# Kernel optimization log

Hardware: AMD Instinct MI355X
Metric: run time of the kernel (lower is better)

## Reference

```python
import jax, jax.numpy as jnp
import numpy as np

EMBED_DIM = 1024
NUM_HEADS = 16
HEAD_DIM = EMBED_DIM // NUM_HEADS
MAX_DIST = 128
NUM_BUCKETS = 2 * MAX_DIST + 1  # 257: fixes off-by-one in original Embedding sizing


def setup_inputs() -> dict:
    key = jax.random.key(0)
    ks = jax.random.split(key, 10)
    B, S, D = 2, 2048, EMBED_DIM
    s = 1.0 / np.sqrt(D)
    return {
        "x": jax.random.normal(ks[0], (B, S, D), dtype=jnp.float32),
        "Wq": jax.random.normal(ks[1], (D, D), dtype=jnp.float32) * s,
        "bq": jnp.zeros((D,), dtype=jnp.float32),
        "Wk": jax.random.normal(ks[2], (D, D), dtype=jnp.float32) * s,
        "bk": jnp.zeros((D,), dtype=jnp.float32),
        "Wv": jax.random.normal(ks[3], (D, D), dtype=jnp.float32) * s,
        "bv": jnp.zeros((D,), dtype=jnp.float32),
        "Wo": jax.random.normal(ks[4], (D, D), dtype=jnp.float32) * s,
        "bo": jnp.zeros((D,), dtype=jnp.float32),
        "rel_emb": jax.random.normal(ks[5], (NUM_BUCKETS, NUM_HEADS), dtype=jnp.float32) * 0.02,
    }


def _rel_bias(rel_emb, seq_len):
    # relative position clamped to [-MAX_DIST, MAX_DIST], shifted to [0, 2*MAX_DIST]
    pos = jnp.arange(seq_len)
    rel = jnp.clip(pos[:, None] - pos[None, :], -MAX_DIST, MAX_DIST) + MAX_DIST
    bias = rel_emb[rel]                    # [S, S, H]
    return jnp.transpose(bias, (2, 0, 1))  # [H, S, S]


def reference(x, Wq, bq, Wk, bk, Wv, bv, Wo, bo, rel_emb):
    B, S, D = x.shape
    H, Hd = NUM_HEADS, HEAD_DIM
    # torch Linear: y = x @ W.T + b
    q = (x @ Wq.T + bq).reshape(B, S, H, Hd).transpose(0, 2, 1, 3)  # [B,H,S,Hd]
    k = (x @ Wk.T + bk).reshape(B, S, H, Hd).transpose(0, 2, 1, 3)
    v = (x @ Wv.T + bv).reshape(B, S, H, Hd).transpose(0, 2, 1, 3)
    scores = jnp.einsum("bhqd,bhkd->bhqk", q, k) / jnp.sqrt(jnp.float32(Hd))
    scores = scores + _rel_bias(rel_emb, S)[None]  # add [H,S,S] bias
    probs = jax.nn.softmax(scores, axis=-1)
    out = jnp.einsum("bhqk,bhkd->bhqd", probs, v)
    out = out.transpose(0, 2, 1, 3).reshape(B, S, D)
    return out @ Wo.T + bo
```

## Files before the change

kernel.cpp:

```cpp
#include <hip/hip_runtime.h>
#include <hip/hip_bf16.h>
#include <cstdint>
#include <cstddef>

#define DEVI __device__ __forceinline__

static constexpr int SEQ = 2048;
static constexpr int DM  = 1024;
static constexpr int NH  = 16;
static constexpr int HD  = 64;
static constexpr int NTOK = 2 * SEQ;
static constexpr int NBUCKET = 257;
static constexpr float LOG2E = 1.44269504088896f;

typedef __attribute__((ext_vector_type(8))) short bf16x8;
typedef __attribute__((ext_vector_type(4))) float f32x4;
#define MFMA16(a, b, c) __builtin_amdgcn_mfma_f32_16x16x32_bf16((a), (b), (c), 0, 0, 0)

DEVI float bf1(uint16_t u)  { return __uint_as_float(((uint32_t)u) << 16); }
DEVI uint16_t f2bf(float f) {
    uint32_t x = __float_as_uint(f);
    x += 0x7fffu + ((x >> 16) & 1u);
    return (uint16_t)(x >> 16);
}
DEVI bf16x8 ld_frag(const uint16_t* p) {
    union { uint4 u; bf16x8 f; } c;
    c.u = *(const uint4*)p;
    return c.f;
}
DEVI void gld16(const uint16_t* g, uint16_t* l) {
    __builtin_amdgcn_global_load_lds(
        (const __attribute__((address_space(1))) uint32_t*)g,
        (__attribute__((address_space(3))) uint32_t*)l, 16, 0, 0);
}

__global__ void sniff_kernel(const uint16_t* __restrict__ x, int* __restrict__ flag)
{
    int bad = 0;
    for (int i = threadIdx.x; i < 512; i += 64) {
        const float v = bf1(x[i]);
        if (!(fabsf(v) < 64.0f)) bad = 1;
    }
    const unsigned long long m = __ballot(bad);
    if (threadIdx.x == 0) *flag = (m != 0ull) ? 1 : 0;
}

__global__ __launch_bounds__(256)
void convert_kernel(const void* __restrict__ x, const void* __restrict__ Wq,
                    const void* __restrict__ Wk, const void* __restrict__ Wv,
                    const void* __restrict__ Wo, const void* __restrict__ bq,
                    const void* __restrict__ bk, const void* __restrict__ bv,
                    const void* __restrict__ bo, uint16_t* __restrict__ dst,
                    const int* __restrict__ flagp)
{
    const bool f32in = (*flagp != 0);
    const size_t M4 = 4194304, M1 = 1048576;
    const size_t e = ((size_t)blockIdx.x * 256 + threadIdx.x) * 8;
    const void* src; size_t off;
    if      (e < M4)                 { src = x;  off = e; }
    else if (e < M4 + M1)            { src = Wq; off = e - M4; }
    else if (e < M4 + 2*M1)          { src = Wk; off = e - M4 - M1; }
    else if (e < M4 + 3*M1)          { src = Wv; off = e - M4 - 2*M1; }
    else if (e < M4 + 4*M1)          { src = Wo; off = e - M4 - 3*M1; }
    else if (e < M4 + 4*M1 + 1024)   { src = bq; off = e - M4 - 4*M1; }
    else if (e < M4 + 4*M1 + 2048)   { src = bk; off = e - M4 - 4*M1 - 1024; }
    else if (e < M4 + 4*M1 + 3072)   { src = bv; off = e - M4 - 4*M1 - 2048; }
    else                             { src = bo; off = e - M4 - 4*M1 - 3072; }
    if (f32in) {
        const float4 a = *(const float4*)((const float*)src + off);
        const float4 b = *(const float4*)((const float*)src + off + 4);
        uint4 o;
        o.x = (uint32_t)f2bf(a.x) | ((uint32_t)f2bf(a.y) << 16);
        o.y = (uint32_t)f2bf(a.z) | ((uint32_t)f2bf(a.w) << 16);
        o.z = (uint32_t)f2bf(b.x) | ((uint32_t)f2bf(b.y) << 16);
        o.w = (uint32_t)f2bf(b.z) | ((uint32_t)f2bf(b.w) << 16);
        *(uint4*)(dst + e) = o;
    } else {
        *(uint4*)(dst + e) = *(const uint4*)((const uint16_t*)src + off);
    }
}

__global__ __launch_bounds__(256)
void gemm_qkv(const uint16_t* __restrict__ xc, const uint16_t* __restrict__ Wqkv,
              const uint16_t* __restrict__ bqkv,
              uint16_t* __restrict__ Qw, uint16_t* __restrict__ Kw,
              uint16_t* __restrict__ Vt)
{
    __shared__ uint16_t As[128 * 32];
    __shared__ uint16_t Bs[128 * 32];
    const int tid = threadIdx.x, bx = blockIdx.x;
    const int lane = tid & 63, wave = tid >> 6;
    const int ln = lane & 15, quad = lane >> 4;
    const int wm = (wave & 1) * 64, wn = (wave >> 1) * 64;

    const uint16_t *Ab, *Bb;
    int bm, bn, vor;
    if (bx < 512) {
        vor = 0; bm = (bx >> 4) * 128; bn = (bx & 15) * 128;
        Ab = xc + (size_t)bm * DM;  Bb = Wqkv + (size_t)bn * DM;
    } else {
        vor = 1; const int b2 = bx - 512; bm = (b2 >> 5) * 128; bn = (b2 & 31) * 128;
        Ab = Wqkv + (size_t)(2048 + bm) * DM;  Bb = xc + (size_t)bn * DM;
    }

    f32x4 acc[4][4];
    #pragma unroll
    for (int i = 0; i < 4; ++i)
        #pragma unroll
        for (int j = 0; j < 4; ++j) acc[i][j] = (f32x4){0.f, 0.f, 0.f, 0.f};

    const int s0 = tid, s1 = 256 + tid;
    const uint16_t* ga0 = Ab + (size_t)(s0 >> 2) * DM + (s0 & 3) * 8;
    const uint16_t* ga1 = Ab + (size_t)(s1 >> 2) * DM + (s1 & 3) * 8;
    const uint16_t* gb0 = Bb + (size_t)(s0 >> 2) * DM + (s0 & 3) * 8;
    const uint16_t* gb1 = Bb + (size_t)(s1 >> 2) * DM + (s1 & 3) * 8;

    for (int k0 = 0; k0 < DM; k0 += 32) {
        __syncthreads();
        gld16(ga0 + k0, &As[s0 * 8]);
        gld16(ga1 + k0, &As[s1 * 8]);
        gld16(gb0 + k0, &Bs[s0 * 8]);
        gld16(gb1 + k0, &Bs[s1 * 8]);
        __syncthreads();

        bf16x8 af[4], bfr[4];
        #pragma unroll
        for (int t = 0; t < 4; ++t) {
            af[t]  = ld_frag(&As[(wm + t * 16 + ln) * 32 + quad * 8]);
            bfr[t] = ld_frag(&Bs[(wn + t * 16 + ln) * 32 + quad * 8]);
        }
        #pragma unroll
        for (int ti = 0; ti < 4; ++ti)
            #pragma unroll
            for (int tj = 0; tj < 4; ++tj)
                acc[ti][tj] = MFMA16(af[ti], bfr[tj], acc[ti][tj]);
    }

    if (!vor) {
        #pragma unroll
        for (int tj = 0; tj < 4; ++tj) {
            const int c = bn + wn + tj * 16 + ln;
            const int mat = c >> 10, h = (c >> 6) & 15, hd = c & 63;
            uint16_t* dstp = mat ? Kw : Qw;
            const float scale = mat ? 1.0f : (0.125f * LOG2E);
            const float bb = bf1(bqkv[c]);
            #pragma unroll
            for (int ti = 0; ti < 4; ++ti)
                #pragma unroll
                for (int r = 0; r < 4; ++r) {
                    const int row = bm + wm + ti * 16 + quad * 4 + r;
                    const int b = row >> 11, s = row & 2047;
                    dstp[(((size_t)b * NH + h) * SEQ + s) * HD + hd] =
                        f2bf((acc[ti][tj][r] + bb) * scale);
                }
        }
    } else {
        #pragma unroll
        for (int ti = 0; ti < 4; ++ti)
            #pragma unroll
            for (int r = 0; r < 4; ++r) {
                const int f = bm + wm + ti * 16 + quad * 4 + r;
                const int h = f >> 6, hd = f & 63;
                const float bb = bf1(bqkv[2048 + f]);
                #pragma unroll
                for (int tj = 0; tj < 4; ++tj) {
                    const int t = bn + wn + tj * 16 + ln;
                    const int b = t >> 11, s = t & 2047;
                    Vt[(((size_t)b * NH + h) * HD + hd) * SEQ + s] = f2bf(acc[ti][tj][r] + bb);
                }
            }
    }
}

__global__ __launch_bounds__(256)
void gemm_out(const uint16_t* __restrict__ Cw, const uint16_t* __restrict__ Woc,
              const uint16_t* __restrict__ boc, void* __restrict__ out,
              const int* __restrict__ flagp)
{
    __shared__ uint16_t As[128 * 32];
    __shared__ uint16_t Bs[64 * 32];
    const int tid = threadIdx.x, bx = blockIdx.x;
    const int lane = tid & 63, wave = tid >> 6;
    const int ln = lane & 15, quad = lane >> 4;
    const int wm = (wave & 1) * 64, wn = (wave >> 1) * 32;
    const int bm = (bx >> 4) * 128, bn = (bx & 15) * 64;
    const uint16_t* Ab = Cw + (size_t)bm * DM;
    const uint16_t* Bb = Woc + (size_t)bn * DM;

    f32x4 acc[4][2];
    #pragma unroll
    for (int i = 0; i < 4; ++i)
        #pragma unroll
        for (int j = 0; j < 2; ++j) acc[i][j] = (f32x4){0.f, 0.f, 0.f, 0.f};

    const int s0 = tid, s1 = 256 + tid;
    const uint16_t* ga0 = Ab + (size_t)(s0 >> 2) * DM + (s0 & 3) * 8;
    const uint16_t* ga1 = Ab + (size_t)(s1 >> 2) * DM + (s1 & 3) * 8;
    const uint16_t* gb0 = Bb + (size_t)(s0 >> 2) * DM + (s0 & 3) * 8;

    for (int k0 = 0; k0 < DM; k0 += 32) {
        __syncthreads();
        gld16(ga0 + k0, &As[s0 * 8]);
        gld16(ga1 + k0, &As[s1 * 8]);
        gld16(gb0 + k0, &Bs[s0 * 8]);
        __syncthreads();

        bf16x8 af[4], bfr[2];
        #pragma unroll
        for (int t = 0; t < 4; ++t)
            af[t] = ld_frag(&As[(wm + t * 16 + ln) * 32 + quad * 8]);
        #pragma unroll
        for (int t = 0; t < 2; ++t)
            bfr[t] = ld_frag(&Bs[(wn + t * 16 + ln) * 32 + quad * 8]);
        #pragma unroll
        for (int ti = 0; ti < 4; ++ti)
            #pragma unroll
            for (int tj = 0; tj < 2; ++tj)
                acc[ti][tj] = MFMA16(af[ti], bfr[tj], acc[ti][tj]);
    }

    const bool f32o = (*flagp != 0);
    #pragma unroll
    for (int tj = 0; tj < 2; ++tj) {
        const int c = bn + wn + tj * 16 + ln;
        const float bb = bf1(boc[c]);
        #pragma unroll
        for (int ti = 0; ti < 4; ++ti)
            #pragma unroll
            for (int r = 0; r < 4; ++r) {
                const int row = bm + wm + ti * 16 + quad * 4 + r;
                const float v = acc[ti][tj][r] + bb;
                if (f32o) ((float*)out)[(size_t)row * DM + c] = v;
                else      ((uint16_t*)out)[(size_t)row * DM + c] = f2bf(v);
            }
    }
}

#define ATTN_COMPUTE(K0, KSB, VSB)                                             \
  do {                                                                         \
    const int mode_ = ((K0) >= q0 + 256) ? 0 : (((K0) + 192 <= q0) ? 2 : 1);   \
    if (mode_ != 1) {                                                          \
      const float binit_ = (mode_ == 0) ? bneg : bpos;                         \
      _Pragma("unroll")                                                        \
      for (int nt = 0; nt < 4; ++nt) {                                         \
        const bf16x8 kf0 = ld_frag((KSB) + kvo[nt][0]);                        \
        const bf16x8 kf1 = ld_frag((KSB) + kvo[nt][1]);                        \
        f32x4 s4 = (f32x4){binit_, binit_, binit_, binit_};                    \
        s4 = MFMA16(kf0, qf0, s4);                                             \
        s4 = MFMA16(kf1, qf1, s4);                                             \
        uint32_t pb[4];                                                        \
        _Pragma("unroll")                                                      \
        for (int r = 0; r < 4; ++r)                                            \
          pb[r] = __float_as_uint(__builtin_amdgcn_exp2f(s4[r]));              \
        const uint2 dw = {__builtin_amdgcn_perm(pb[1], pb[0], 0x07060302u),    \
                          __builtin_amdgcn_perm(pb[3], pb[2], 0x07060302u)};   \
        *(uint2*)Pw[nt] = dw;                                                  \
      }                                                                        \
    } else {                                                                   \
      const int iq_ = q0 + wave * 16 + ln + 128 - (K0) - quad * 4;             \
      _Pragma("unroll")                                                        \
      for (int nt = 0; nt < 4; ++nt) {                                         \
        const bf16x8 kf0 = ld_frag((KSB) + kvo[nt][0]);                        \
        const bf16x8 kf1 = ld_frag((KSB) + kvo[nt][1]);                        \
        f32x4 s4 = (f32x4){0.f, 0.f, 0.f, 0.f};                                \
        s4 = MFMA16(kf0, qf0, s4);                                             \
        s4 = MFMA16(kf1, qf1, s4);                                             \
        uint32_t pb[4];                                                        \
        _Pragma("unroll")                                                      \
        for (int r = 0; r < 4; ++r) {                                          \
          int x_ = iq_ - (nt * 16 + r);                                        \
          x_ = max(0, min(256, x_));                                           \
          pb[r] = __float_as_uint(__builtin_amdgcn_exp2f(s4[r] + bias_s[x_])); \
        }                                                                      \
        const uint2 dw = {__builtin_amdgcn_perm(pb[1], pb[0], 0x07060302u),    \
                          __builtin_amdgcn_perm(pb[3], pb[2], 0x07060302u)};   \
        *(uint2*)Pw[nt] = dw;                                                  \
      }                                                                        \
    }                                                                          \
    const bf16x8 pf0 = ld_frag(pfp0);                                          \
    const bf16x8 pf1 = ld_frag(pfp1);                                          \
    lf = MFMA16(pf0, onef, lf);                                                \
    lf = MFMA16(pf1, onef, lf);                                                \
    _Pragma("unroll")                                                          \
    for (int dt = 0; dt < 4; ++dt) {                                           \
      o[dt] = MFMA16(pf0, ld_frag((VSB) + kvo[dt][0]), o[dt]);                 \
      o[dt] = MFMA16(pf1, ld_frag((VSB) + kvo[dt][1]), o[dt]);                 \
    }                                                                          \
  } while (0)

__global__ __launch_bounds__(512, 4)
void attn_mfma(const uint16_t* __restrict__ Q, const uint16_t* __restrict__ K,
               const uint16_t* __restrict__ Vt, const void* __restrict__ rel,
               uint16_t* __restrict__ ctx, const int* __restrict__ flagp)
{
    __shared__ alignas(16) uint16_t Ks[2][64 * 64];
    __shared__ alignas(16) uint16_t Vls[2][64 * 64];
    __shared__ alignas(16) uint16_t Pl[8][16 * 64];
    __shared__ float bias_s[NBUCKET];

    const bool f32in = (*flagp != 0);
    const int tid = threadIdx.x, wave = tid >> 6, lane = tid & 63;
    const int ln = lane & 15, quad = lane >> 4;

    const int blk = blockIdx.x;
    const int bh = (blk & 7) * 4 + ((blk >> 3) & 3);
    const int qt = blk >> 5;
    const int b = bh >> 4, h = bh & 15;
    const int q0 = qt * 128;

    const float C8 = 8.0f * LOG2E;
    for (int i = tid; i < NBUCKET; i += 512) {
        const float bv = f32in ? ((const float*)rel)[i * NH + h]
                               : bf1(((const uint16_t*)rel)[i * NH + h]);
        bias_s[i] = bv * LOG2E - C8;
    }

    const uint16_t* qp = Q + ((size_t)bh * SEQ + q0 + wave * 16 + ln) * HD;
    const bf16x8 qf0 = ld_frag(qp + quad * 8);
    const bf16x8 qf1 = ld_frag(qp + 32 + quad * 8);

    union { uint4 u; bf16x8 f; } onec;
    onec.u = (uint4){0x3F803F80u, 0x3F803F80u, 0x3F803F80u, 0x3F803F80u};
    const bf16x8 onef = onec.f;

    f32x4 o[4];
    f32x4 lf = (f32x4){0.f, 0.f, 0.f, 0.f};
    #pragma unroll
    for (int dt = 0; dt < 4; ++dt) o[dt] = (f32x4){0.f, 0.f, 0.f, 0.f};

    const int swz = ln & 7;
    uint16_t* myP = Pl[wave];

    const int r_ = tid >> 3, c_ = (tid & 7) ^ (r_ & 7);
    const int koff = r_ * HD + c_ * 8;
    const int voff = r_ * SEQ + c_ * 8;
    uint16_t* const kd0 = &Ks[0][tid * 8];
    uint16_t* const kd1 = &Ks[1][tid * 8];
    uint16_t* const vd0 = &Vls[0][tid * 8];
    uint16_t* const vd1 = &Vls[1][tid * 8];

    const uint16_t* kg = K  + (size_t)bh * SEQ * HD + koff;
    const uint16_t* vg = Vt + (size_t)bh * HD * SEQ + voff;

    int kvo[4][2];
    #pragma unroll
    for (int t = 0; t < 4; ++t) {
        const int row = (t * 16 + ln) * 64;
        kvo[t][0] = row + ((0 + quad) ^ swz) * 8;
        kvo[t][1] = row + ((4 + quad) ^ swz) * 8;
    }
    uint16_t* Pw[4];
    #pragma unroll
    for (int nt = 0; nt < 4; ++nt) {
        const int cb = (2 * nt + (quad >> 1)) ^ swz;
        Pw[nt] = &myP[ln * 64 + cb * 8 + (quad & 1) * 4];
    }
    const uint16_t* const pfp0 = &myP[ln * 64 + ((0 + quad) ^ swz) * 8];
    const uint16_t* const pfp1 = &myP[ln * 64 + ((4 + quad) ^ swz) * 8];

    gld16(kg, kd0); gld16(vg, vd0);
    kg += 64 * HD; vg += 64;
    __syncthreads();
    const float bneg = bias_s[0], bpos = bias_s[256];

    for (int t = 0; t < 16; ++t) {
        gld16(kg, kd1); gld16(vg, vd1);
        kg += 64 * HD; vg += 64;
        ATTN_COMPUTE(t * 128, &Ks[0][0], &Vls[0][0]);
        __syncthreads();

        if (t < 15) {
            gld16(kg, kd0); gld16(vg, vd0);
            kg += 64 * HD; vg += 64;
        }
        ATTN_COMPUTE(t * 128 + 64, &Ks[1][0], &Vls[1][0]);
        __syncthreads();
    }

    #pragma unroll
    for (int r = 0; r < 4; ++r) {
        const float inv = 1.0f / lf[r];
        const int qq = q0 + wave * 16 + quad * 4 + r;
        #pragma unroll
        for (int dt = 0; dt < 4; ++dt)
            ctx[(((size_t)b * SEQ + qq) * NH + h) * HD + dt * 16 + ln] =
                f2bf(o[dt][r] * inv);
    }
}

extern "C" void kernel_launch(void* const* d_in, const int* in_sizes, int n_in,
                              void* d_out, int out_size, void* d_ws, size_t ws_size,
                              hipStream_t stream)
{
    const void* x   = d_in[0];
    const void* Wq  = d_in[1];
    const void* bq  = d_in[2];
    const void* Wk  = d_in[3];
    const void* bk  = d_in[4];
    const void* Wv  = d_in[5];
    const void* bv  = d_in[6];
    const void* Wo  = d_in[7];
    const void* bo  = d_in[8];
    const void* rel = d_in[9];

    const size_t M4 = 4194304, M1 = 1048576;
    uint16_t* ws16 = (uint16_t*)d_ws;
    uint16_t* xc   = ws16;
    uint16_t* Wqkv = ws16 + M4;
    uint16_t* Woc  = ws16 + M4 + 3 * M1;
    uint16_t* bqkv = ws16 + M4 + 4 * M1;
    uint16_t* boc  = bqkv + 3072;
    uint16_t* Qw   = ws16 + M4 + 4 * M1 + 8192;
    uint16_t* Kw   = Qw + M4;
    uint16_t* Vt   = Kw + M4;
    int* flag = (int*)(Vt + M4);
    uint16_t* Cw = xc;

    sniff_kernel<<<1, 64, 0, stream>>>((const uint16_t*)x, flag);
    convert_kernel<<<4098, 256, 0, stream>>>(x, Wq, Wk, Wv, Wo, bq, bk, bv, bo,
                                             ws16, flag);
    gemm_qkv<<<768, 256, 0, stream>>>(xc, Wqkv, bqkv, Qw, Kw, Vt);
    attn_mfma<<<512, 512, 0, stream>>>(Qw, Kw, Vt, rel, Cw, flag);
    gemm_out<<<512, 256, 0, stream>>>(Cw, Woc, boc, d_out, flag);
}
```

Baseline: 207.4 us.

## Process two query sub-tiles per wave to reuse K/V fragments in attention

The attention block drops from 8 waves to 4, and each wave now handles 32 query rows as two 16-row groups. Every K and V fragment read from shared memory feeds two MFMAs instead of one, which halves LDS fragment traffic per unit of work. Each thread now issues two global-to-LDS copies per tile, since fewer threads remain to stage it. The cost is roughly double the accumulator and Q registers per wave and fewer waves per block, which may reduce latency hiding.

```diff
diff --git a/kernel.cpp b/kernel.cpp
--- a/kernel.cpp
+++ b/kernel.cpp
@@ -245,57 +245,72 @@
       for (int nt = 0; nt < 4; ++nt) {                                         \
         const bf16x8 kf0 = ld_frag((KSB) + kvo[nt][0]);                        \
         const bf16x8 kf1 = ld_frag((KSB) + kvo[nt][1]);                        \
-        f32x4 s4 = (f32x4){binit_, binit_, binit_, binit_};                    \
-        s4 = MFMA16(kf0, qf0, s4);                                             \
-        s4 = MFMA16(kf1, qf1, s4);                                             \
-        uint32_t pb[4];                                                        \
         _Pragma("unroll")                                                      \
-        for (int r = 0; r < 4; ++r)                                            \
-          pb[r] = __float_as_uint(__builtin_amdgcn_exp2f(s4[r]));              \
-        const uint2 dw = {__builtin_amdgcn_perm(pb[1], pb[0], 0x07060302u),    \
-                          __builtin_amdgcn_perm(pb[3], pb[2], 0x07060302u)};   \
-        *(uint2*)Pw[nt] = dw;                                                  \
+        for (int qg = 0; qg < 2; ++qg) {                                       \
+          f32x4 s4 = (f32x4){binit_, binit_, binit_, binit_};                  \
+          s4 = MFMA16(kf0, qf0[qg], s4);                                       \
+          s4 = MFMA16(kf1, qf1[qg], s4);                                       \
+          uint32_t pb[4];                                                      \
+          _Pragma("unroll")                                                    \
+          for (int r = 0; r < 4; ++r)                                          \
+            pb[r] = __float_as_uint(__builtin_amdgcn_exp2f(s4[r]));            \
+          const uint2 dw = {__builtin_amdgcn_perm(pb[1], pb[0], 0x07060302u),  \
+                            __builtin_amdgcn_perm(pb[3], pb[2], 0x07060302u)}; \
+          *(uint2*)Pw[qg][nt] = dw;                                            \
+        }                                                                      \
       }                                                                        \
     } else {                                                                   \
-      const int iq_ = q0 + wave * 16 + ln + 128 - (K0) - quad * 4;             \
       _Pragma("unroll")                                                        \
       for (int nt = 0; nt < 4; ++nt) {                                         \
         const bf16x8 kf0 = ld_frag((KSB) + kvo[nt][0]);                        \
         const bf16x8 kf1 = ld_frag((KSB) + kvo[nt][1]);                        \
-        f32x4 s4 = (f32x4){0.f, 0.f, 0.f, 0.f};                                \
-        s4 = MFMA16(kf0, qf0, s4);                                             \
-        s4 = MFMA16(kf1, qf1, s4);                                             \
-        uint32_t pb[4];                                                        \
         _Pragma("unroll")                                                      \
-        for (int r = 0; r < 4; ++r) {                                          \
-          int x_ = iq_ - (nt * 16 + r);                                        \
-          x_ = max(0, min(256, x_));                                           \
-          pb[r] = __float_as_uint(__builtin_amdgcn_exp2f(s4[r] + bias_s[x_])); \
+        for (int qg = 0; qg < 2; ++qg) {                                       \
+          const int iq_ = q0 + wave * 32 + qg * 16 + ln + 128 - (K0) - quad * 4;\
+          f32x4 s4 = (f32x4){0.f, 0.f, 0.f, 0.f};                              \
+          s4 = MFMA16(kf0, qf0[qg], s4);                                       \
+          s4 = MFMA16(kf1, qf1[qg], s4);                                       \
+          uint32_t pb[4];                                                      \
+          _Pragma("unroll")                                                    \
+          for (int r = 0; r < 4; ++r) {                                        \
+            int x_ = iq_ - (nt * 16 + r);                                      \
+            x_ = max(0, min(256, x_));                                         \
+            pb[r] = __float_as_uint(__builtin_amdgcn_exp2f(s4[r] + bias_s[x_]));\
+          }                                                                    \
+          const uint2 dw = {__builtin_amdgcn_perm(pb[1], pb[0], 0x07060302u),  \
+                            __builtin_amdgcn_perm(pb[3], pb[2], 0x07060302u)}; \
+          *(uint2*)Pw[qg][nt] = dw;                                            \
         }                                                                      \
-        const uint2 dw = {__builtin_amdgcn_perm(pb[1], pb[0], 0x07060302u),    \
-                          __builtin_amdgcn_perm(pb[3], pb[2], 0x07060302u)};   \
-        *(uint2*)Pw[nt] = dw;                                                  \
       }                                                                        \
     }                                                                          \
-    const bf16x8 pf0 = ld_frag(pfp0);                                          \
-    const bf16x8 pf1 = ld_frag(pfp1);                                          \
-    lf = MFMA16(pf0, onef, lf);                                                \
-    lf = MFMA16(pf1, onef, lf);                                                \
+    bf16x8 pfa[2], pfb[2];                                                     \
+    _Pragma("unroll")                                                          \
+    for (int qg = 0; qg < 2; ++qg) {                                           \
+      pfa[qg] = ld_frag(pfp[qg][0]);                                           \
+      pfb[qg] = ld_frag(pfp[qg][1]);                                           \
+      lf[qg] = MFMA16(pfa[qg], onef, lf[qg]);                                  \
+      lf[qg] = MFMA16(pfb[qg], onef, lf[qg]);                                  \
+    }                                                                          \
     _Pragma("unroll")                                                          \
     for (int dt = 0; dt < 4; ++dt) {                                           \
-      o[dt] = MFMA16(pf0, ld_frag((VSB) + kvo[dt][0]), o[dt]);                 \
-      o[dt] = MFMA16(pf1, ld_frag((VSB) + kvo[dt][1]), o[dt]);                 \
+      const bf16x8 vfa = ld_frag((VSB) + kvo[dt][0]);                          \
+      const bf16x8 vfb = ld_frag((VSB) + kvo[dt][1]);                          \
+      _Pragma("unroll")                                                        \
+      for (int qg = 0; qg < 2; ++qg) {                                         \
+        o[qg][dt] = MFMA16(pfa[qg], vfa, o[qg][dt]);                           \
+        o[qg][dt] = MFMA16(pfb[qg], vfb, o[qg][dt]);                           \
+      }                                                                        \
     }                                                                          \
   } while (0)
 
-__global__ __launch_bounds__(512, 4)
+__global__ __launch_bounds__(256, 2)
 void attn_mfma(const uint16_t* __restrict__ Q, const uint16_t* __restrict__ K,
                const uint16_t* __restrict__ Vt, const void* __restrict__ rel,
                uint16_t* __restrict__ ctx, const int* __restrict__ flagp)
 {
     __shared__ alignas(16) uint16_t Ks[2][64 * 64];
     __shared__ alignas(16) uint16_t Vls[2][64 * 64];
-    __shared__ alignas(16) uint16_t Pl[8][16 * 64];
+    __shared__ alignas(16) uint16_t Pl[4][32 * 64];
     __shared__ float bias_s[NBUCKET];
 
     const bool f32in = (*flagp != 0);
@@ -309,38 +324,53 @@
     const int q0 = qt * 128;
 
     const float C8 = 8.0f * LOG2E;
-    for (int i = tid; i < NBUCKET; i += 512) {
+    for (int i = tid; i < NBUCKET; i += 256) {
         const float bv = f32in ? ((const float*)rel)[i * NH + h]
                                : bf1(((const uint16_t*)rel)[i * NH + h]);
         bias_s[i] = bv * LOG2E - C8;
     }
 
-    const uint16_t* qp = Q + ((size_t)bh * SEQ + q0 + wave * 16 + ln) * HD;
-    const bf16x8 qf0 = ld_frag(qp + quad * 8);
-    const bf16x8 qf1 = ld_frag(qp + 32 + quad * 8);
+    bf16x8 qf0[2], qf1[2];
+    #pragma unroll
+    for (int qg = 0; qg < 2; ++qg) {
+        const uint16_t* qp =
+            Q + ((size_t)bh * SEQ + q0 + wave * 32 + qg * 16 + ln) * HD;
+        qf0[qg] = ld_frag(qp + quad * 8);
+        qf1[qg] = ld_frag(qp + 32 + quad * 8);
+    }
 
     union { uint4 u; bf16x8 f; } onec;
     onec.u = (uint4){0x3F803F80u, 0x3F803F80u, 0x3F803F80u, 0x3F803F80u};
     const bf16x8 onef = onec.f;
 
-    f32x4 o[4];
-    f32x4 lf = (f32x4){0.f, 0.f, 0.f, 0.f};
-    #pragma unroll
-    for (int dt = 0; dt < 4; ++dt) o[dt] = (f32x4){0.f, 0.f, 0.f, 0.f};
+    f32x4 o[2][4];
+    f32x4 lf[2];
+    #pragma unroll
+    for (int qg = 0; qg < 2; ++qg) {
+        lf[qg] = (f32x4){0.f, 0.f, 0.f, 0.f};
+        #pragma unroll
+        for (int dt = 0; dt < 4; ++dt) o[qg][dt] = (f32x4){0.f, 0.f, 0.f, 0.f};
+    }
 
     const int swz = ln & 7;
     uint16_t* myP = Pl[wave];
 
-    const int r_ = tid >> 3, c_ = (tid & 7) ^ (r_ & 7);
-    const int koff = r_ * HD + c_ * 8;
-    const int voff = r_ * SEQ + c_ * 8;
-    uint16_t* const kd0 = &Ks[0][tid * 8];
-    uint16_t* const kd1 = &Ks[1][tid * 8];
-    uint16_t* const vd0 = &Vls[0][tid * 8];
-    uint16_t* const vd1 = &Vls[1][tid * 8];
-
-    const uint16_t* kg = K  + (size_t)bh * SEQ * HD + koff;
-    const uint16_t* vg = Vt + (size_t)bh * HD * SEQ + voff;
+    const int s0_ = tid, s1_ = tid + 256;
+    const int r0_ = s0_ >> 3, c0_ = (s0_ & 7) ^ (r0_ & 7);
+    const int r1_ = s1_ >> 3, c1_ = (s1_ & 7) ^ (r1_ & 7);
+    const int koff0 = r0_ * HD + c0_ * 8,  koff1 = r1_ * HD + c1_ * 8;
+    const int voff0 = r0_ * SEQ + c0_ * 8, voff1 = r1_ * SEQ + c1_ * 8;
+    uint16_t* const kd00 = &Ks[0][s0_ * 8];
+    uint16_t* const kd01 = &Ks[0][s1_ * 8];
+    uint16_t* const kd10 = &Ks[1][s0_ * 8];
+    uint16_t* const kd11 = &Ks[1][s1_ * 8];
+    uint16_t* const vd00 = &Vls[0][s0_ * 8];
+    uint16_t* const vd01 = &Vls[0][s1_ * 8];
+    uint16_t* const vd10 = &Vls[1][s0_ * 8];
+    uint16_t* const vd11 = &Vls[1][s1_ * 8];
+
+    const uint16_t* kg = K  + (size_t)bh * SEQ * HD;
+    const uint16_t* vg = Vt + (size_t)bh * HD * SEQ;
 
     int kvo[4][2];
     #pragma unroll
@@ -349,28 +379,36 @@
         kvo[t][0] = row + ((0 + quad) ^ swz) * 8;
         kvo[t][1] = row + ((4 + quad) ^ swz) * 8;
     }
-    uint16_t* Pw[4];
-    #pragma unroll
-    for (int nt = 0; nt < 4; ++nt) {
-        const int cb = (2 * nt + (quad >> 1)) ^ swz;
-        Pw[nt] = &myP[ln * 64 + cb * 8 + (quad & 1) * 4];
-    }
-    const uint16_t* const pfp0 = &myP[ln * 64 + ((0 + quad) ^ swz) * 8];
-    const uint16_t* const pfp1 = &myP[ln * 64 + ((4 + quad) ^ swz) * 8];
-
-    gld16(kg, kd0); gld16(vg, vd0);
+    uint16_t* Pw[2][4];
+    const uint16_t* pfp[2][2];
+    #pragma unroll
+    for (int qg = 0; qg < 2; ++qg) {
+        const int prow = (qg * 16 + ln) * 64;
+        #pragma unroll
+        for (int nt = 0; nt < 4; ++nt) {
+            const int cb = (2 * nt + (quad >> 1)) ^ swz;
+            Pw[qg][nt] = &myP[prow + cb * 8 + (quad & 1) * 4];
+        }
+        pfp[qg][0] = &myP[prow + ((0 + quad) ^ swz) * 8];
+        pfp[qg][1] = &myP[prow + ((4 + quad) ^ swz) * 8];
+    }
+
+    gld16(kg + koff0, kd00); gld16(kg + koff1, kd01);
+    gld16(vg + voff0, vd00); gld16(vg + voff1, vd01);
     kg += 64 * HD; vg += 64;
     __syncthreads();
     const float bneg = bias_s[0], bpos = bias_s[256];
 
     for (int t = 0; t < 16; ++t) {
-        gld16(kg, kd1); gld16(vg, vd1);
+        gld16(kg + koff0, kd10); gld16(kg + koff1, kd11);
+        gld16(vg + voff0, vd10); gld16(vg + voff1, vd11);
         kg += 64 * HD; vg += 64;
         ATTN_COMPUTE(t * 128, &Ks[0][0], &Vls[0][0]);
         __syncthreads();
 
         if (t < 15) {
-            gld16(kg, kd0); gld16(vg, vd0);
+            gld16(kg + koff0, kd00); gld16(kg + koff1, kd01);
+            gld16(vg + voff0, vd00); gld16(vg + voff1, vd01);
             kg += 64 * HD; vg += 64;
         }
         ATTN_COMPUTE(t * 128 + 64, &Ks[1][0], &Vls[1][0]);
@@ -378,14 +416,16 @@
     }
 
     #pragma unroll
-    for (int r = 0; r < 4; ++r) {
-        const float inv = 1.0f / lf[r];
-        const int qq = q0 + wave * 16 + quad * 4 + r;
-        #pragma unroll
-        for (int dt = 0; dt < 4; ++dt)
-            ctx[(((size_t)b * SEQ + qq) * NH + h) * HD + dt * 16 + ln] =
-                f2bf(o[dt][r] * inv);
-    }
+    for (int qg = 0; qg < 2; ++qg)
+        #pragma unroll
+        for (int r = 0; r < 4; ++r) {
+            const float inv = 1.0f / lf[qg][r];
+            const int qq = q0 + wave * 32 + qg * 16 + quad * 4 + r;
+            #pragma unroll
+            for (int dt = 0; dt < 4; ++dt)
+                ctx[(((size_t)b * SEQ + qq) * NH + h) * HD + dt * 16 + ln] =
+                    f2bf(o[qg][dt][r] * inv);
+        }
 }
 
 extern "C" void kernel_launch(void* const* d_in, const int* in_sizes, int n_in,
@@ -420,6 +460,6 @@
     convert_kernel<<<4098, 256, 0, stream>>>(x, Wq, Wk, Wv, Wo, bq, bk, bv, bo,
                                              ws16, flag);
     gemm_qkv<<<768, 256, 0, stream>>>(xc, Wqkv, bqkv, Qw, Kw, Vt);
-    attn_mfma<<<512, 512, 0, stream>>>(Qw, Kw, Vt, rel, Cw, flag);
+    attn_mfma<<<512, 256, 0, stream>>>(Qw, Kw, Vt, rel, Cw, flag);
     gemm_out<<<512, 256, 0, stream>>>(Cw, Woc, boc, d_out, flag);
 }
```

Result: no change. 205.7 us (-0.8%).
